# Kernel tuning notes

Measured on AMD Instinct MI355X. Metric: run time of the kernel, lower is better.

Reference implementation:

```python
import jax, jax.numpy as jnp
import numpy as np

N = 20000   # nodes
E = 320000  # edges (avg degree 16)
K = 3       # Chebyshev order


def _glorot(key, shape):
    fan_in, fan_out = shape[-2], shape[-1]
    lim = (6.0 / (fan_in + fan_out)) ** 0.5
    return jax.random.uniform(key, shape, minval=-lim, maxval=lim, dtype=jnp.float32)


def setup_inputs() -> dict:
    key = jax.random.key(0)
    ks = jax.random.split(key, 8)
    v = jax.random.normal(ks[0], (N, 86), dtype=jnp.float32)
    edges = jax.random.randint(ks[1], (2, E), 0, N, dtype=jnp.int32)
    W1 = _glorot(ks[2], (K, 86, 128));  b1 = jnp.zeros((128,), jnp.float32)
    W2 = _glorot(ks[3], (K, 128, 256)); b2 = jnp.zeros((256,), jnp.float32)
    W3 = _glorot(ks[4], (K, 256, 512)); b3 = jnp.zeros((512,), jnp.float32)
    return {"v": v, "edges": edges, "W1": W1, "b1": b1,
            "W2": W2, "b2": b2, "W3": W3, "b3": b3}


def _cheb_norm(edges, n):
    # PyG ChebConv with sym norm, lambda_max=2: L_hat = L - I = -D^-1/2 A D^-1/2
    # (diagonal entries from get_laplacian (+1) and add_self_loops (-1) cancel).
    # Self loops are removed before computing the Laplacian -> mask them out.
    row, col = edges[0], edges[1]
    w = (row != col).astype(jnp.float32)
    deg = jax.ops.segment_sum(w, row, num_segments=n)
    dinv = jnp.where(deg > 0, jax.lax.rsqrt(jnp.maximum(deg, 1e-12)), 0.0)
    norm_w = -dinv[row] * w * dinv[col]  # [E]
    return row, col, norm_w


def _cheb_conv(x, row, col, norm_w, W, b):
    # W: [K, in, out]
    def prop(z):  # L_hat @ z via edge gather + segment scatter-add
        return jax.ops.segment_sum(norm_w[:, None] * z[col], row, num_segments=x.shape[0])
    Tx0 = x
    out = Tx0 @ W[0]
    Tx1 = prop(Tx0)
    out = out + Tx1 @ W[1]
    Tx2 = 2.0 * prop(Tx1) - Tx0
    out = out + Tx2 @ W[2]
    return out + b


def reference(v, edges, W1, b1, W2, b2, W3, b3):
    row, col, norm_w = _cheb_norm(edges, v.shape[0])
    nk = jax.random.key(42)
    x1 = jax.nn.relu(_cheb_conv(v, row, col, norm_w, W1, b1))
    x1 = x1 * jax.random.normal(jax.random.fold_in(nk, 1), x1.shape, x1.dtype)
    x2 = jax.nn.relu(_cheb_conv(x1, row, col, norm_w, W2, b2))
    x2 = x2 * jax.random.normal(jax.random.fold_in(nk, 2), x2.shape, x2.dtype)
    x3 = jax.nn.relu(_cheb_conv(x2, row, col, norm_w, W3, b3))
    x3 = x3 * jax.random.normal(jax.random.fold_in(nk, 3), x3.shape, x3.dtype)
    return (x1, x2, x3)
```

## Files before the change

kernel.cpp:

```cpp
#include <hip/hip_runtime.h>
#include <stdint.h>
#include <math.h>

#define DEV static __device__ __forceinline__

typedef __attribute__((ext_vector_type(8))) short bf16x8;
typedef __attribute__((ext_vector_type(4))) float f32x4;
typedef __attribute__((ext_vector_type(8))) unsigned short u16x8;
typedef __attribute__((ext_vector_type(2))) unsigned int u32x2;
typedef __attribute__((ext_vector_type(4))) unsigned int u32x4;

DEV uint32_t rotl32(uint32_t v, int d) { return (v << d) | (v >> (32 - d)); }

DEV void threefry2x32(uint32_t k0, uint32_t k1, uint32_t& x0, uint32_t& x1) {
  const uint32_t k2 = k0 ^ k1 ^ 0x1BD11BDAu;
  x0 += k0; x1 += k1;
#define TFR(R) { x0 += x1; x1 = rotl32(x1, R) ^ x0; }
  TFR(13) TFR(15) TFR(26) TFR(6)
  x0 += k1; x1 += k2 + 1u;
  TFR(17) TFR(29) TFR(16) TFR(24)
  x0 += k2; x1 += k0 + 2u;
  TFR(13) TFR(15) TFR(26) TFR(6)
  x0 += k0; x1 += k1 + 3u;
  TFR(17) TFR(29) TFR(16) TFR(24)
  x0 += k1; x1 += k2 + 4u;
  TFR(13) TFR(15) TFR(26) TFR(6)
  x0 += k2; x1 += k0 + 5u;
#undef TFR
}

DEV float erfinv_f32(float x) {
  float w = -log1pf(-x * x);
  float p;
  if (w < 5.0f) {
    w -= 2.5f;
    p = 2.81022636e-08f;
    p = fmaf(p, w, 3.43273939e-07f);
    p = fmaf(p, w, -3.5233877e-06f);
    p = fmaf(p, w, -4.39150654e-06f);
    p = fmaf(p, w, 0.00021858087f);
    p = fmaf(p, w, -0.00125372503f);
    p = fmaf(p, w, -0.00417768164f);
    p = fmaf(p, w, 0.246640727f);
    p = fmaf(p, w, 1.50140941f);
  } else {
    w = sqrtf(w) - 3.0f;
    p = -0.000200214257f;
    p = fmaf(p, w, 0.000100950558f);
    p = fmaf(p, w, 0.00134934322f);
    p = fmaf(p, w, -0.00367342844f);
    p = fmaf(p, w, 0.00573950773f);
    p = fmaf(p, w, -0.0076224613f);
    p = fmaf(p, w, 0.00943887047f);
    p = fmaf(p, w, 1.00167406f);
    p = fmaf(p, w, 2.83297682f);
  }
  return p * x;
}

DEV float normal_from_bits(uint32_t bits) {
  float f = __uint_as_float((bits >> 9) | 0x3F800000u) - 1.0f;
  const float lo = -0.99999994f;
  float u = fmaf(f, 2.0f, lo);
  u = fmaxf(u, lo);
  return 1.41421356f * erfinv_f32(u);
}

DEV unsigned short f2bf(float f) {
  uint32_t u = __float_as_uint(f);
  uint32_t r = u + 0x7FFFu + ((u >> 16) & 1u);
  return (unsigned short)(r >> 16);
}

DEV float bf2f(uint32_t h) { return __uint_as_float(h << 16); }

DEV float4 noise4(uint32_t f0, uint32_t f1, uint32_t i4) {
  uint32_t base = i4 * 4u;
  float4 r;
  { uint32_t a = 0u, b = base + 0u; threefry2x32(f0, f1, a, b); r.x = normal_from_bits(a ^ b); }
  { uint32_t a = 0u, b = base + 1u; threefry2x32(f0, f1, a, b); r.y = normal_from_bits(a ^ b); }
  { uint32_t a = 0u, b = base + 2u; threefry2x32(f0, f1, a, b); r.z = normal_from_bits(a ^ b); }
  { uint32_t a = 0u, b = base + 3u; threefry2x32(f0, f1, a, b); r.w = normal_from_bits(a ^ b); }
  return r;
}

DEV void noise_fill(unsigned short* __restrict__ nb, int n4_begin, int n4_end, int fold,
                    int gbase, int gstride) {
  uint32_t f0k = 0u, f1k = (uint32_t)fold;
  threefry2x32(0u, 42u, f0k, f1k);
  for (int i4 = n4_begin + gbase; i4 < n4_end; i4 += gstride) {
    float4 r = noise4(f0k, f1k, (uint32_t)i4);
    u32x2 u;
    u.x = (uint32_t)f2bf(r.x) | ((uint32_t)f2bf(r.y) << 16);
    u.y = (uint32_t)f2bf(r.z) | ((uint32_t)f2bf(r.w) << 16);
    __builtin_nontemporal_store(u, (u32x2*)&nb[(size_t)i4 * 4]);
  }
}

__global__ void count_kernel(const int* __restrict__ rows, const int* __restrict__ cols,
                             int* __restrict__ counts, int* __restrict__ degs, int E) {
  int e = blockIdx.x * blockDim.x + threadIdx.x;
  if (e < E) {
    int r = rows[e];
    atomicAdd(&counts[r], 1);
    if (r != cols[e]) atomicAdd(&degs[r], 1);
  }
}

#define SCAN_T 1024
__global__ __launch_bounds__(SCAN_T) void scan_kernel(const int* __restrict__ counts,
                                                      int* __restrict__ row_ptr,
                                                      int* __restrict__ cursor, int N) {
  __shared__ int sa[SCAN_T], sb[SCAN_T];
  const int t = threadIdx.x;
  const int CH = (N + SCAN_T - 1) / SCAN_T;
  int base = t * CH;
  int psum = 0;
  for (int k = 0; k < CH; ++k) {
    int idx = base + k;
    if (idx < N) psum += counts[idx];
  }
  sa[t] = psum;
  __syncthreads();
  int* src = sa; int* dst = sb;
  for (int off = 1; off < SCAN_T; off <<= 1) {
    int v = src[t];
    if (t >= off) v += src[t - off];
    dst[t] = v;
    __syncthreads();
    int* tmp = src; src = dst; dst = tmp;
  }
  int running = src[t] - psum;
  for (int k = 0; k < CH; ++k) {
    int idx = base + k;
    if (idx < N) {
      row_ptr[idx] = running;
      cursor[idx] = running;
      running += counts[idx];
    }
  }
  if (t == SCAN_T - 1) row_ptr[N] = running;
}

__global__ void fill_kernel(const int* __restrict__ rows, const int* __restrict__ cols,
                            const int* __restrict__ degs, int* __restrict__ cursor,
                            float2* __restrict__ ecv, int E) {
  int e = blockIdx.x * blockDim.x + threadIdx.x;
  if (e < E) {
    int r = rows[e], c = cols[e];
    int dr = degs[r], dc = degs[c];
    float w = (r != c && dr > 0 && dc > 0) ? -rsqrtf((float)dr) * rsqrtf((float)dc) : 0.0f;
    int pos = atomicAdd(&cursor[r], 1);
    ecv[pos] = make_float2(__int_as_float(c), w);
  }
}

__global__ void prep_kernel(const float* __restrict__ v,
                            const float* __restrict__ W1, const float* __restrict__ W2,
                            const float* __restrict__ W3,
                            unsigned short* __restrict__ vb, unsigned short* __restrict__ wt1,
                            unsigned short* __restrict__ wt2, unsigned short* __restrict__ wt3,
                            int N) {
  int i = blockIdx.x * 256 + threadIdx.x;
  int nv = N * 96;
  if (i < nv) {
    int r = i / 96, k = i % 96;
    vb[i] = (k < 86) ? f2bf(v[(size_t)r * 86 + k]) : (unsigned short)0;
    return;
  }
  i -= nv;
  if (i < 3 * 128 * 96) {
    int k = i % 96, o = (i / 96) % 128, p = i / (96 * 128);
    float val = 0.0f;
    if (k < 86) {
      if (p == 0)      val = W1[((size_t)0 * 86 + k) * 128 + o] - W1[((size_t)2 * 86 + k) * 128 + o];
      else if (p == 1) val = W1[((size_t)1 * 86 + k) * 128 + o];
      else             val = 2.0f * W1[((size_t)2 * 86 + k) * 128 + o];
    }
    wt1[i] = (k < 86) ? f2bf(val) : (unsigned short)0;
    return;
  }
  i -= 3 * 128 * 96;
  if (i < 3 * 256 * 128) {
    int k = i % 128, o = (i / 128) % 256, p = i / (128 * 256);
    float val;
    if (p == 0)      val = W2[((size_t)0 * 128 + k) * 256 + o] - W2[((size_t)2 * 128 + k) * 256 + o];
    else if (p == 1) val = W2[((size_t)1 * 128 + k) * 256 + o];
    else             val = 2.0f * W2[((size_t)2 * 128 + k) * 256 + o];
    wt2[i] = f2bf(val);
    return;
  }
  i -= 3 * 256 * 128;
  if (i < 3 * 512 * 256) {
    int k = i % 256, o = (i / 256) % 512, p = i / (256 * 512);
    float val;
    if (p == 0)      val = W3[((size_t)0 * 256 + k) * 512 + o] - W3[((size_t)2 * 256 + k) * 512 + o];
    else if (p == 1) val = W3[((size_t)1 * 256 + k) * 512 + o];
    else             val = 2.0f * W3[((size_t)2 * 256 + k) * 512 + o];
    wt3[i] = f2bf(val);
  }
}

DEV void ld8(const unsigned short* __restrict__ base, size_t off, float* v) {
  uint4 u = *(const uint4*)(base + off);
  v[0] = bf2f(u.x & 0xffffu); v[1] = bf2f(u.x >> 16);
  v[2] = bf2f(u.y & 0xffffu); v[3] = bf2f(u.y >> 16);
  v[4] = bf2f(u.z & 0xffffu); v[5] = bf2f(u.z >> 16);
  v[6] = bf2f(u.w & 0xffffu); v[7] = bf2f(u.w >> 16);
}

DEV void gather_node(const int* __restrict__ row_ptr, const float2* __restrict__ ecv,
                     const unsigned short* __restrict__ xsrc, int sstride, int fl,
                     int node, float* acc) {
  const int s = row_ptr[node], e = row_ptr[node + 1];
  int j = s;
  for (; j + 8 <= e; j += 8) {
    float2 cw[8];
    float vv[8][8];
#pragma unroll
    for (int q = 0; q < 8; ++q) cw[q] = ecv[j + q];
#pragma unroll
    for (int q = 0; q < 8; ++q)
      ld8(xsrc, (size_t)__float_as_int(cw[q].x) * sstride + fl, vv[q]);
#pragma unroll
    for (int q = 0; q < 8; ++q)
#pragma unroll
      for (int z = 0; z < 8; ++z) acc[z] = fmaf(cw[q].y, vv[q][z], acc[z]);
  }
  for (; j + 2 <= e; j += 2) {
    float2 cw[2];
    float vv[2][8];
#pragma unroll
    for (int q = 0; q < 2; ++q) cw[q] = ecv[j + q];
#pragma unroll
    for (int q = 0; q < 2; ++q)
      ld8(xsrc, (size_t)__float_as_int(cw[q].x) * sstride + fl, vv[q]);
#pragma unroll
    for (int q = 0; q < 2; ++q)
#pragma unroll
      for (int z = 0; z < 8; ++z) acc[z] = fmaf(cw[q].y, vv[q][z], acc[z]);
  }
  for (; j < e; ++j) {
    float2 cw = ecv[j];
    float vv[8];
    ld8(xsrc, (size_t)__float_as_int(cw.x) * sstride + fl, vv);
#pragma unroll
    for (int z = 0; z < 8; ++z) acc[z] = fmaf(cw.y, vv[z], acc[z]);
  }
}

DEV void store8(unsigned short* __restrict__ outb, size_t ob, const float* acc) {
  u32x4 u;
  u.x = (uint32_t)f2bf(acc[0]) | ((uint32_t)f2bf(acc[1]) << 16);
  u.y = (uint32_t)f2bf(acc[2]) | ((uint32_t)f2bf(acc[3]) << 16);
  u.z = (uint32_t)f2bf(acc[4]) | ((uint32_t)f2bf(acc[5]) << 16);
  u.w = (uint32_t)f2bf(acc[6]) | ((uint32_t)f2bf(acc[7]) << 16);
  __builtin_nontemporal_store(u, (u32x4*)&outb[ob]);
}

template <int LPN, int NL, int FOLD>
__global__ __launch_bounds__(256) void gather_prop(
    const int* __restrict__ row_ptr, const float2* __restrict__ ecv,
    const unsigned short* __restrict__ xsrc, int sstride,
    unsigned short* __restrict__ outb, int N, int Fpad,
    unsigned short* __restrict__ nbuf, int n4_begin, int n4_end) {
  const int wave = threadIdx.x >> 6, lane = threadIdx.x & 63;
  const int sub = lane / LPN;
  const int fl = (lane - sub * LPN) * 8;
  const int node = (blockIdx.x * 4 + wave) * NL + sub;
  if (sub < NL && node < N && fl < Fpad) {
    float acc[8] = {};
    gather_node(row_ptr, ecv, xsrc, sstride, fl, node, acc);
    store8(outb, (size_t)node * Fpad + fl, acc);
  }
  noise_fill(nbuf, n4_begin, n4_end, FOLD, blockIdx.x * 256 + (int)threadIdx.x, gridDim.x * 256);
}

template <int G, int FOLD>
__global__ __launch_bounds__(256) void gather_prop_sl(
    const int* __restrict__ row_ptr, const float2* __restrict__ ecv,
    const unsigned short* __restrict__ xsrc, int sstride,
    unsigned short* __restrict__ outb, int N, int Fpad, int NBK,
    unsigned short* __restrict__ nbuf, int n4_begin, int n4_end) {
  const int flat = blockIdx.x;
  const int xcd = flat & 7, j = flat >> 3;
  const int slice = xcd / G;
  const int nb = j * G + (xcd % G);
  if (nb < NBK) {
    const int wave = threadIdx.x >> 6, lane = threadIdx.x & 63;
    const int sub = lane >> 3;
    const int fl = slice * 64 + (lane & 7) * 8;
    const int node = nb * 32 + wave * 8 + sub;
    if (node < N) {
      float acc[8] = {};
      gather_node(row_ptr, ecv, xsrc, sstride, fl, node, acc);
      store8(outb, (size_t)node * Fpad + fl, acc);
    }
  }
  noise_fill(nbuf, n4_begin, n4_end, FOLD, flat * 256 + (int)threadIdx.x, gridDim.x * 256);
}

template <int BM, int FPAD, int KS, int OB>
__global__ __launch_bounds__(512, 4) void gemm3_db(
    const unsigned short* __restrict__ A0, const unsigned short* __restrict__ A1,
    const unsigned short* __restrict__ A2,
    const unsigned short* __restrict__ Wt, const float* __restrict__ bias,
    const unsigned short* __restrict__ noise,
    int M, int MT, int O, float* __restrict__ out, unsigned short* __restrict__ outb,
    int obstride) {
  constexpr int BN = 128;
  constexpr int NSP = FPAD / KS;
  constexpr int NSTEP = 3 * NSP;
  constexpr int CPR = KS / 8;
  constexpr int LST = KS + 8;
  constexpr int NA = BM * CPR;
  constexpr int NB = BN * CPR;
  constexpr int ACH = (NA + 511) / 512;
  constexpr int BCH = (NB + 511) / 512;
  constexpr int MFR = BM / 32;
  constexpr int KK = KS / 32;

  const int flat = blockIdx.x;
  const int xcd = flat & 7, idx = flat >> 3;
  const int mtile = xcd + 8 * (idx / OB);
  const int obl = idx - (idx / OB) * OB;
  if (mtile >= MT) return;
  const int bm = mtile * BM;
  const int bo = obl * BN;

  __shared__ unsigned short sA[2][BM * LST];
  __shared__ unsigned short sB[2][BN * LST];

  const int tid = threadIdx.x;
  const int lane = tid & 63;
  const int wave = tid >> 6;
  const int wm = wave >> 2, wo = wave & 3;
  const int l15 = lane & 15;
  const int kg = (lane >> 4) * 8;

  f32x4 acc[MFR][2] = {};
  const unsigned short* As[3] = {A0, A1, A2};

  u16x8 ra0[ACH], rb0[BCH], ra1[ACH], rb1[BCH];

  auto issue = [&](int s, u16x8 (&ra)[ACH], u16x8 (&rb)[BCH]) {
    int p = s / NSP, k0 = (s % NSP) * KS;
    const unsigned short* __restrict__ A = As[p];
    const unsigned short* __restrict__ B = Wt + (size_t)p * O * FPAD;
#pragma unroll
    for (int c = 0; c < ACH; ++c) {
      int idx2 = tid + c * 512;
      if (NA % 512 == 0 || idx2 < NA) {
        int row = idx2 / CPR, ch = (idx2 % CPR) * 8;
        int gm = bm + row; if (gm >= M) gm = M - 1;
        ra[c] = *(const u16x8*)(A + (size_t)gm * FPAD + k0 + ch);
      }
    }
#pragma unroll
    for (int c = 0; c < BCH; ++c) {
      int idx2 = tid + c * 512;
      if (NB % 512 == 0 || idx2 < NB) {
        int row = idx2 / CPR, ch = (idx2 % CPR) * 8;
        rb[c] = *(const u16x8*)(B + (size_t)(bo + row) * FPAD + k0 + ch);
      }
    }
  };

  auto lds_write = [&](int buf, u16x8 (&ra)[ACH], u16x8 (&rb)[BCH]) {
#pragma unroll
    for (int c = 0; c < ACH; ++c) {
      int idx2 = tid + c * 512;
      if (NA % 512 == 0 || idx2 < NA) {
        int row = idx2 / CPR, ch = (idx2 % CPR) * 8;
        *(u16x8*)&sA[buf][row * LST + ch] = ra[c];
      }
    }
#pragma unroll
    for (int c = 0; c < BCH; ++c) {
      int idx2 = tid + c * 512;
      if (NB % 512 == 0 || idx2 < NB) {
        int row = idx2 / CPR, ch = (idx2 % CPR) * 8;
        *(u16x8*)&sB[buf][row * LST + ch] = rb[c];
      }
    }
  };

  auto compute = [&](int buf) {
#pragma unroll
    for (int kk = 0; kk < KK; ++kk) {
      bf16x8 af[MFR], bfr[2];
#pragma unroll
      for (int mi = 0; mi < MFR; ++mi)
        af[mi] = *(const bf16x8*)&sA[buf][(wm * (BM / 2) + mi * 16 + l15) * LST + kk * 32 + kg];
#pragma unroll
      for (int ni = 0; ni < 2; ++ni)
        bfr[ni] = *(const bf16x8*)&sB[buf][(wo * 32 + ni * 16 + l15) * LST + kk * 32 + kg];
#pragma unroll
      for (int mi = 0; mi < MFR; ++mi)
#pragma unroll
        for (int ni = 0; ni < 2; ++ni)
          acc[mi][ni] = __builtin_amdgcn_mfma_f32_16x16x32_bf16(af[mi], bfr[ni], acc[mi][ni], 0, 0, 0);
    }
  };

  issue(0, ra0, rb0);
  issue(1, ra1, rb1);
  lds_write(0, ra0, rb0);
  __syncthreads();

#pragma unroll
  for (int s = 0; s < NSTEP; ++s) {
    if ((s & 1) == 0) {
      if (s + 2 < NSTEP) issue(s + 2, ra0, rb0);
      compute(s & 1);
      if (s + 1 < NSTEP) { lds_write((s + 1) & 1, ra1, rb1); __syncthreads(); }
    } else {
      if (s + 2 < NSTEP) issue(s + 2, ra1, rb1);
      compute(s & 1);
      if (s + 1 < NSTEP) { lds_write((s + 1) & 1, ra0, rb0); __syncthreads(); }
    }
  }

  const int r0 = (lane >> 4) * 4;
#pragma unroll
  for (int mi = 0; mi < MFR; ++mi) {
#pragma unroll
    for (int r = 0; r < 4; ++r) {
      int gm = bm + wm * (BM / 2) + mi * 16 + r0 + r;
      if (gm >= M) continue;
#pragma unroll
      for (int ni = 0; ni < 2; ++ni) {
        int go = bo + wo * 32 + ni * 16 + l15;
        float vv = acc[mi][ni][r] + bias[go];
        vv = vv > 0.0f ? vv : 0.0f;
        float res = vv * bf2f((uint32_t)noise[(size_t)gm * O + go]);
        __builtin_nontemporal_store(res, &out[(size_t)gm * O + go]);
        if (outb)
          __builtin_nontemporal_store((unsigned short)f2bf(res),
                                      &outb[(size_t)gm * obstride + go]);
      }
    }
  }
}

extern "C" void kernel_launch(void* const* d_in, const int* in_sizes, int n_in,
                              void* d_out, int out_size, void* d_ws, size_t ws_size,
                              hipStream_t stream) {
  const float* v    = (const float*)d_in[0];
  const int*  edges = (const int*)d_in[1];
  const float* W1 = (const float*)d_in[2];
  const float* b1 = (const float*)d_in[3];
  const float* W2 = (const float*)d_in[4];
  const float* b2 = (const float*)d_in[5];
  const float* W3 = (const float*)d_in[6];
  const float* b3 = (const float*)d_in[7];
  float* out = (float*)d_out;

  const int N = in_sizes[0] / 86;
  const int E = in_sizes[1] / 2;
  const int* rows = edges;
  const int* cols = edges + E;

  uintptr_t cur = (uintptr_t)d_ws;
  auto alloc = [&](size_t bytes) {
    cur = (cur + 15) & ~(uintptr_t)15;
    void* p = (void*)cur;
    cur += bytes;
    return p;
  };
  float2* ecv          = (float2*)alloc((size_t)E * 8);
  int* counts          = (int*)alloc((size_t)N * 4);
  int* degs            = (int*)alloc((size_t)N * 4);
  int* row_ptr         = (int*)alloc((size_t)(N + 1) * 4);
  int* cursor          = (int*)alloc((size_t)N * 4);
  unsigned short* tx1b = (unsigned short*)alloc((size_t)N * 256 * 2);
  unsigned short* tx2b = (unsigned short*)alloc((size_t)N * 256 * 2);
  unsigned short* vb   = (unsigned short*)alloc((size_t)N * 96 * 2);
  unsigned short* x1b  = (unsigned short*)alloc((size_t)N * 128 * 2);
  unsigned short* x2b  = (unsigned short*)alloc((size_t)N * 256 * 2);
  unsigned short* wt1  = (unsigned short*)alloc((size_t)3 * 128 * 96 * 2);
  unsigned short* wt2  = (unsigned short*)alloc((size_t)3 * 256 * 128 * 2);
  unsigned short* wt3  = (unsigned short*)alloc((size_t)3 * 512 * 256 * 2);
  unsigned short* nb2  = (unsigned short*)alloc((size_t)N * 256 * 2);
  unsigned short* nb3  = (unsigned short*)alloc((size_t)N * 512 * 2);
  unsigned short* nb1  = nb3;

  float* x1 = out;
  float* x2 = x1 + (size_t)N * 128;
  float* x3 = x2 + (size_t)N * 256;

  hipMemsetAsync(counts, 0, (size_t)2 * N * sizeof(int), stream);
  count_kernel<<<(E + 255) / 256, 256, 0, stream>>>(rows, cols, counts, degs, E);
  scan_kernel<<<1, SCAN_T, 0, stream>>>(counts, row_ptr, cursor, N);
  fill_kernel<<<(E + 255) / 256, 256, 0, stream>>>(rows, cols, degs, cursor, ecv, E);
  {
    int total = N * 96 + 3 * 128 * 96 + 3 * 256 * 128 + 3 * 512 * 256;
    prep_kernel<<<(total + 255) / 256, 256, 0, stream>>>(v, W1, W2, W3, vb, wt1, wt2, wt3, N);
  }

  const int NBK = (N + 31) / 32;

  {
    int pb = (N + 15) / 16;
    int t4 = N * 128 / 4, h4 = t4 / 2;
    gather_prop<12, 4, 1><<<pb, 256, 0, stream>>>(row_ptr, ecv, vb, 96, tx1b, N, 96, nb1, 0, h4);
    gather_prop<12, 4, 1><<<pb, 256, 0, stream>>>(row_ptr, ecv, tx1b, 96, tx2b, N, 96, nb1, h4, t4);
    int mt = (N + 63) / 64;
    int grid = 8 * ((mt + 7) / 8) * 1;
    gemm3_db<64, 96, 32, 1><<<grid, 512, 0, stream>>>(vb, tx1b, tx2b, wt1, b1, nb1,
                                                      N, mt, 128, x1, x1b, 128);
  }
  {
    int pgrid = 8 * ((NBK + 3) / 4);
    int t4 = N * 256 / 4, h4 = t4 / 2;
    gather_prop_sl<4, 2><<<pgrid, 256, 0, stream>>>(row_ptr, ecv, x1b, 128, tx1b, N, 128, NBK, nb2, 0, h4);
    gather_prop_sl<4, 2><<<pgrid, 256, 0, stream>>>(row_ptr, ecv, tx1b, 128, tx2b, N, 128, NBK, nb2, h4, t4);
    int mt = (N + 127) / 128;
    int grid = 8 * ((mt + 7) / 8) * 2;
    gemm3_db<128, 128, 64, 2><<<grid, 512, 0, stream>>>(x1b, tx1b, tx2b, wt2, b2, nb2,
                                                        N, mt, 256, x2, x2b, 256);
  }
  {
    int pgrid = 8 * ((NBK + 1) / 2);
    int t4 = N * 512 / 4, h4 = t4 / 2;
    gather_prop_sl<2, 3><<<pgrid, 256, 0, stream>>>(row_ptr, ecv, x2b, 256, tx1b, N, 256, NBK, nb3, 0, h4);
    gather_prop_sl<2, 3><<<pgrid, 256, 0, stream>>>(row_ptr, ecv, tx1b, 256, tx2b, N, 256, NBK, nb3, h4, t4);
    int mt = (N + 127) / 128;
    int grid = 8 * ((mt + 7) / 8) * 4;
    gemm3_db<128, 256, 64, 4><<<grid, 512, 0, stream>>>(x2b, tx1b, tx2b, wt3, b3, nb3,
                                                        N, mt, 512, x3, nullptr, 0);
  }
}
```

Before: 403.8 us.

## Drop XCD feature-sliced gather kernel and use plain stores everywhere

Removes the gather_prop_sl kernel, which split feature columns across XCDs so that each XCD's L2 would hold only one slice of the source features. Layers 2 and 3 now use the generic gather_prop kernel, where each node's full feature row is handled by one group of lanes. All nontemporal stores (noise fill, gather outputs, GEMM epilogue) become ordinary stores, so freshly written intermediates can stay in cache for the next kernel. The tradeoff is that every XCD's L2 now gathers from the whole feature matrix, giving up the per-XCD locality that the slicing provided.

```diff
diff --git a/kernel.cpp b/kernel.cpp
--- a/kernel.cpp
+++ b/kernel.cpp
@@ -93,7 +93,7 @@
     u32x2 u;
     u.x = (uint32_t)f2bf(r.x) | ((uint32_t)f2bf(r.y) << 16);
     u.y = (uint32_t)f2bf(r.z) | ((uint32_t)f2bf(r.w) << 16);
-    __builtin_nontemporal_store(u, (u32x2*)&nb[(size_t)i4 * 4]);
+    *(u32x2*)&nb[(size_t)i4 * 4] = u;
   }
 }
 
@@ -255,7 +255,7 @@
   u.y = (uint32_t)f2bf(acc[2]) | ((uint32_t)f2bf(acc[3]) << 16);
   u.z = (uint32_t)f2bf(acc[4]) | ((uint32_t)f2bf(acc[5]) << 16);
   u.w = (uint32_t)f2bf(acc[6]) | ((uint32_t)f2bf(acc[7]) << 16);
-  __builtin_nontemporal_store(u, (u32x4*)&outb[ob]);
+  *(u32x4*)&outb[ob] = u;
 }
 
 template <int LPN, int NL, int FOLD>
@@ -274,30 +274,6 @@
     store8(outb, (size_t)node * Fpad + fl, acc);
   }
   noise_fill(nbuf, n4_begin, n4_end, FOLD, blockIdx.x * 256 + (int)threadIdx.x, gridDim.x * 256);
-}
-
-template <int G, int FOLD>
-__global__ __launch_bounds__(256) void gather_prop_sl(
-    const int* __restrict__ row_ptr, const float2* __restrict__ ecv,
-    const unsigned short* __restrict__ xsrc, int sstride,
-    unsigned short* __restrict__ outb, int N, int Fpad, int NBK,
-    unsigned short* __restrict__ nbuf, int n4_begin, int n4_end) {
-  const int flat = blockIdx.x;
-  const int xcd = flat & 7, j = flat >> 3;
-  const int slice = xcd / G;
-  const int nb = j * G + (xcd % G);
-  if (nb < NBK) {
-    const int wave = threadIdx.x >> 6, lane = threadIdx.x & 63;
-    const int sub = lane >> 3;
-    const int fl = slice * 64 + (lane & 7) * 8;
-    const int node = nb * 32 + wave * 8 + sub;
-    if (node < N) {
-      float acc[8] = {};
-      gather_node(row_ptr, ecv, xsrc, sstride, fl, node, acc);
-      store8(outb, (size_t)node * Fpad + fl, acc);
-    }
-  }
-  noise_fill(nbuf, n4_begin, n4_end, FOLD, flat * 256 + (int)threadIdx.x, gridDim.x * 256);
 }
 
 template <int BM, int FPAD, int KS, int OB>
@@ -434,10 +410,8 @@
         float vv = acc[mi][ni][r] + bias[go];
         vv = vv > 0.0f ? vv : 0.0f;
         float res = vv * bf2f((uint32_t)noise[(size_t)gm * O + go]);
-        __builtin_nontemporal_store(res, &out[(size_t)gm * O + go]);
-        if (outb)
-          __builtin_nontemporal_store((unsigned short)f2bf(res),
-                                      &outb[(size_t)gm * obstride + go]);
+        out[(size_t)gm * O + go] = res;
+        if (outb) outb[(size_t)gm * obstride + go] = f2bf(res);
       }
     }
   }
@@ -498,8 +472,6 @@
     prep_kernel<<<(total + 255) / 256, 256, 0, stream>>>(v, W1, W2, W3, vb, wt1, wt2, wt3, N);
   }
 
-  const int NBK = (N + 31) / 32;
-
   {
     int pb = (N + 15) / 16;
     int t4 = N * 128 / 4, h4 = t4 / 2;
@@ -511,20 +483,20 @@
                                                       N, mt, 128, x1, x1b, 128);
   }
   {
-    int pgrid = 8 * ((NBK + 3) / 4);
+    int pb = (N + 15) / 16;
     int t4 = N * 256 / 4, h4 = t4 / 2;
-    gather_prop_sl<4, 2><<<pgrid, 256, 0, stream>>>(row_ptr, ecv, x1b, 128, tx1b, N, 128, NBK, nb2, 0, h4);
-    gather_prop_sl<4, 2><<<pgrid, 256, 0, stream>>>(row_ptr, ecv, tx1b, 128, tx2b, N, 128, NBK, nb2, h4, t4);
+    gather_prop<16, 4, 2><<<pb, 256, 0, stream>>>(row_ptr, ecv, x1b, 128, tx1b, N, 128, nb2, 0, h4);
+    gather_prop<16, 4, 2><<<pb, 256, 0, stream>>>(row_ptr, ecv, tx1b, 128, tx2b, N, 128, nb2, h4, t4);
     int mt = (N + 127) / 128;
     int grid = 8 * ((mt + 7) / 8) * 2;
     gemm3_db<128, 128, 64, 2><<<grid, 512, 0, stream>>>(x1b, tx1b, tx2b, wt2, b2, nb2,
                                                         N, mt, 256, x2, x2b, 256);
   }
   {
-    int pgrid = 8 * ((NBK + 1) / 2);
+    int pb = (N + 7) / 8;
     int t4 = N * 512 / 4, h4 = t4 / 2;
-    gather_prop_sl<2, 3><<<pgrid, 256, 0, stream>>>(row_ptr, ecv, x2b, 256, tx1b, N, 256, NBK, nb3, 0, h4);
-    gather_prop_sl<2, 3><<<pgrid, 256, 0, stream>>>(row_ptr, ecv, tx1b, 256, tx2b, N, 256, NBK, nb3, h4, t4);
+    gather_prop<32, 2, 3><<<pb, 256, 0, stream>>>(row_ptr, ecv, x2b, 256, tx1b, N, 256, nb3, 0, h4);
+    gather_prop<32, 2, 3><<<pb, 256, 0, stream>>>(row_ptr, ecv, tx1b, 256, tx2b, N, 256, nb3, h4, t4);
     int mt = (N + 127) / 128;
     int grid = 8 * ((mt + 7) / 8) * 4;
     gemm3_db<128, 256, 64, 4><<<grid, 512, 0, stream>>>(x2b, tx1b, tx2b, wt3, b3, nb3,
```

After: 357.4 us. 11.5% less time.
